# Optimization experiments

Hardware: AMD Instinct MI355X
Metric: run time of the kernel (lower is better)

The kernel has to match this reference:

```python
import jax, jax.numpy as jnp
import numpy as np

NUM_HEADS = 12
LOCAL_WINDOW = 7


def setup_inputs() -> dict:
    key = jax.random.key(0)
    k1, k2, k3 = jax.random.split(key, 3)
    B, N, C = 2, 2048, 768
    x = jax.random.normal(k1, (B, N, C), dtype=jnp.float32)
    w_qkv = jax.random.normal(k2, (3 * C, C), dtype=jnp.float32) * (C ** -0.5)
    w_proj = jax.random.normal(k3, (C, C), dtype=jnp.float32) * (C ** -0.5)
    b_proj = jnp.zeros((C,), dtype=jnp.float32)
    return {"x": x, "w_qkv": w_qkv, "w_proj": w_proj, "b_proj": b_proj}


def reference(x, w_qkv, w_proj, b_proj):
    B, N, C = x.shape
    H = NUM_HEADS
    Dh = C // H
    scale = Dh ** -0.5
    # local-window additive mask: 0 within |i-j|<=w, -inf outside (vectorized)
    idx = jnp.arange(N)
    local_mask = jnp.where(
        jnp.abs(idx[:, None] - idx[None, :]) <= LOCAL_WINDOW, 0.0, -jnp.inf
    ).astype(x.dtype)
    qkv = x @ w_qkv.T
    qkv = qkv.reshape(B, N, 3, H, Dh).transpose(2, 0, 3, 1, 4)
    q, k, v = qkv[0], qkv[1], qkv[2]
    attn = jnp.einsum("bhnd,bhmd->bhnm", q, k) * scale
    attn = attn + local_mask[None, None, :, :]
    attn = jax.nn.softmax(attn, axis=-1)
    out = jnp.einsum("bhnm,bhmd->bhnd", attn, v)
    out = out.transpose(0, 2, 1, 3).reshape(B, N, C)
    return out @ w_proj.T + b_proj
```

## Files before the change

### kernel.cpp

```cpp
#include <hip/hip_runtime.h>
#include <hip/hip_bf16.h>

typedef __bf16 bf16;
typedef bf16 bf16x4 __attribute__((ext_vector_type(4)));
typedef bf16 bf16x8 __attribute__((ext_vector_type(8)));
typedef float floatx4 __attribute__((ext_vector_type(4)));

#define GLOBAL_AS __attribute__((address_space(1)))
#define LDS_AS __attribute__((address_space(3)))

__global__ __launch_bounds__(256)
void cvt3_f32_bf16(const float* __restrict__ s0, const float* __restrict__ s1,
                   const float* __restrict__ s2, bf16* __restrict__ d0,
                   bf16* __restrict__ d1, bf16* __restrict__ d2,
                   int n0, int n1, int n2)
{
    int t = blockIdx.x * blockDim.x + threadIdx.x;
    const float* s; bf16* d; int i;
    if (t < n0)                { s = s0; d = d0; i = t; }
    else if (t < n0 + n1)      { s = s1; d = d1; i = t - n0; }
    else if (t < n0 + n1 + n2) { s = s2; d = d2; i = t - n0 - n1; }
    else return;
    float4 v = ((const float4*)s)[i];
    bf16x4 o = { (bf16)v.x, (bf16)v.y, (bf16)v.z, (bf16)v.w };
    ((bf16x4*)d)[i] = o;
}

template<typename CT, bool AF32, bool WF32, int TM, int M, int N, int K,
         int LDA, int LDC>
__global__ __launch_bounds__(256, 2)
void gemm_bt(const void* __restrict__ Av, const void* __restrict__ Wv,
             CT* __restrict__ C, const float* __restrict__ bias)
{
    constexpr int MI = TM / 32;
    __shared__ __align__(16) bf16 As[TM * 32];
    __shared__ __align__(16) bf16 Bs[128 * 32];

    const int tid  = threadIdx.x;
    const int lane = tid & 63;
    const int wave = tid >> 6;
    const int row0 = blockIdx.x * TM;
    const int col0 = blockIdx.y * 128;

    const int wm = (wave & 1) * (TM / 2);
    const int wn = (wave >> 1) * 64;

    floatx4 acc[MI][4] = {};

    const int fr = lane & 15;
    const int fk = (lane >> 4) * 8;

    const int lr = lane >> 2;
    const int lk = (lane & 3) * 8;

    for (int k0 = 0; k0 < K; k0 += 32) {
        if (AF32) {
            constexpr int NV = TM * 4;
            #pragma unroll
            for (int c = 0; c < NV / 256; ++c) {
                const int idx = tid + c * 256;
                const int r   = idx >> 2;
                const int cb  = (idx & 3) * 8;
                const float4* g = (const float4*)((const float*)Av
                                   + (size_t)(row0 + r) * LDA + k0 + cb);
                float4 g0 = g[0], g1 = g[1];
                bf16x8 va;
                va[0]=(bf16)g0.x; va[1]=(bf16)g0.y; va[2]=(bf16)g0.z; va[3]=(bf16)g0.w;
                va[4]=(bf16)g1.x; va[5]=(bf16)g1.y; va[6]=(bf16)g1.z; va[7]=(bf16)g1.w;
                *(bf16x8*)(As + r * 32 + cb) = va;
            }
        } else {
            constexpr int CAW = TM / 64;
            #pragma unroll
            for (int c = 0; c < CAW; ++c) {
                const int chunk = wave * CAW + c;
                const int r = chunk * 16 + lr;
                const bf16* gA = (const bf16*)Av + (size_t)(row0 + r) * LDA + k0 + lk;
                __builtin_amdgcn_global_load_lds((const GLOBAL_AS void*)gA,
                                                 (LDS_AS void*)(As + chunk * 512),
                                                 16, 0, 0);
            }
        }
        if (WF32) {
            #pragma unroll
            for (int c = 0; c < 2; ++c) {
                const int idx = tid + c * 256;
                const int r   = idx >> 2;
                const int cb  = (idx & 3) * 8;
                const float4* g = (const float4*)((const float*)Wv
                                   + (size_t)(col0 + r) * K + k0 + cb);
                float4 g0 = g[0], g1 = g[1];
                bf16x8 vw;
                vw[0]=(bf16)g0.x; vw[1]=(bf16)g0.y; vw[2]=(bf16)g0.z; vw[3]=(bf16)g0.w;
                vw[4]=(bf16)g1.x; vw[5]=(bf16)g1.y; vw[6]=(bf16)g1.z; vw[7]=(bf16)g1.w;
                *(bf16x8*)(Bs + r * 32 + cb) = vw;
            }
        } else {
            #pragma unroll
            for (int c = 0; c < 2; ++c) {
                const int chunk = wave * 2 + c;
                const int r = chunk * 16 + lr;
                const bf16* gB = (const bf16*)Wv + (size_t)(col0 + r) * K + k0 + lk;
                __builtin_amdgcn_global_load_lds((const GLOBAL_AS void*)gB,
                                                 (LDS_AS void*)(Bs + chunk * 512),
                                                 16, 0, 0);
            }
        }
        __syncthreads();

        bf16x8 af[MI], bfr[4];
        #pragma unroll
        for (int i = 0; i < MI; ++i)
            af[i]  = *(const bf16x8*)(As + (wm + i * 16 + fr) * 32 + fk);
        #pragma unroll
        for (int j = 0; j < 4; ++j)
            bfr[j] = *(const bf16x8*)(Bs + (wn + j * 16 + fr) * 32 + fk);
        #pragma unroll
        for (int i = 0; i < MI; ++i)
            #pragma unroll
            for (int j = 0; j < 4; ++j)
                acc[i][j] = __builtin_amdgcn_mfma_f32_16x16x32_bf16(
                    af[i], bfr[j], acc[i][j], 0, 0, 0);

        __syncthreads();
    }

    const int fc  = lane & 15;
    const int fr4 = (lane >> 4) * 4;
    #pragma unroll
    for (int i = 0; i < MI; ++i) {
        #pragma unroll
        for (int j = 0; j < 4; ++j) {
            const int col = col0 + wn + j * 16 + fc;
            const float b = bias ? bias[col] : 0.0f;
            #pragma unroll
            for (int r = 0; r < 4; ++r) {
                const int row = row0 + wm + i * 16 + fr4 + r;
                C[(size_t)row * LDC + col] = (CT)(acc[i][j][r] + b);
            }
        }
    }
}

__global__ __launch_bounds__(256)
void attn_tile(const bf16* __restrict__ qkv, bf16* __restrict__ aout)
{
    __shared__ __align__(16) bf16 Ks[4][32][72];
    __shared__ __align__(16) bf16 Vt[4][64][40];
    __shared__ __align__(16) bf16 Ps[4][16][40];

    const int w    = threadIdx.x >> 6;
    const int lane = threadIdx.x & 63;
    const int c    = lane & 15;
    const int q    = lane >> 4;
    const int wid  = blockIdx.x * 4 + w;
    const int it   = wid & 127;
    const int bh   = wid >> 7;
    const int h    = bh % 12;
    const int b    = bh / 12;
    const int I0   = it * 16;
    const int bbase = b * 2048;
    const int j0   = I0 - 7;

    #pragma unroll
    for (int itr = 0; itr < 4; ++itr) {
        int idx = itr * 64 + lane;
        int row = idx >> 3;
        int dc  = (idx & 7) * 8;
        int jc  = j0 + row; jc = jc < 0 ? 0 : (jc > 2047 ? 2047 : jc);
        const bf16* base = qkv + (size_t)(bbase + jc) * 2304 + h * 64 + dc;
        bf16x8 kv = *(const bf16x8*)(base + 768);
        bf16x8 vv = *(const bf16x8*)(base + 1536);
        *(bf16x8*)(&Ks[w][row][dc]) = kv;
        #pragma unroll
        for (int e = 0; e < 8; ++e) Vt[w][dc + e][row] = vv[e];
    }

    const bf16* qrow = qkv + (size_t)(bbase + I0 + c) * 2304 + h * 64;
    bf16x8 aq0 = *(const bf16x8*)(qrow + q * 8);
    bf16x8 aq1 = *(const bf16x8*)(qrow + 32 + q * 8);

    __syncthreads();

    floatx4 st[2] = {};
    #pragma unroll
    for (int t = 0; t < 2; ++t) {
        bf16x8 k0 = *(const bf16x8*)(&Ks[w][t * 16 + c][q * 8]);
        bf16x8 k1 = *(const bf16x8*)(&Ks[w][t * 16 + c][32 + q * 8]);
        st[t] = __builtin_amdgcn_mfma_f32_16x16x32_bf16(aq0, k0, st[t], 0, 0, 0);
        st[t] = __builtin_amdgcn_mfma_f32_16x16x32_bf16(aq1, k1, st[t], 0, 0, 0);
    }

    float s[2][4];
    #pragma unroll
    for (int t = 0; t < 2; ++t)
        #pragma unroll
        for (int r = 0; r < 4; ++r) {
            int il = q * 4 + r;
            int jl = t * 16 + c;
            int ja = j0 + jl;
            bool valid = (jl >= il) && (jl <= il + 14) && (ja >= 0) && (ja < 2048);
            s[t][r] = valid ? st[t][r] * 0.125f : -1e30f;
        }

    float l[4], p[2][4];
    #pragma unroll
    for (int r = 0; r < 4; ++r) {
        float m2 = fmaxf(s[0][r], s[1][r]);
        #pragma unroll
        for (int mk = 1; mk < 16; mk <<= 1) m2 = fmaxf(m2, __shfl_xor(m2, mk, 64));
        p[0][r] = __expf(s[0][r] - m2);
        p[1][r] = __expf(s[1][r] - m2);
        float l2 = p[0][r] + p[1][r];
        #pragma unroll
        for (int mk = 1; mk < 16; mk <<= 1) l2 += __shfl_xor(l2, mk, 64);
        l[r] = l2;
    }

    #pragma unroll
    for (int r = 0; r < 4; ++r) {
        Ps[w][q * 4 + r][c]      = (bf16)p[0][r];
        Ps[w][q * 4 + r][16 + c] = (bf16)p[1][r];
    }
    __syncthreads();

    bf16x8 ap = *(const bf16x8*)(&Ps[w][c][q * 8]);
    floatx4 ov[4];
    #pragma unroll
    for (int nt = 0; nt < 4; ++nt) {
        bf16x8 vf = *(const bf16x8*)(&Vt[w][nt * 16 + c][q * 8]);
        floatx4 z = {};
        ov[nt] = __builtin_amdgcn_mfma_f32_16x16x32_bf16(ap, vf, z, 0, 0, 0);
    }

    float rl[4];
    #pragma unroll
    for (int r = 0; r < 4; ++r) rl[r] = 1.0f / l[r];
    #pragma unroll
    for (int r = 0; r < 4; ++r) {
        bf16* orow = aout + (size_t)(bbase + I0 + q * 4 + r) * 768 + h * 64;
        #pragma unroll
        for (int nt = 0; nt < 4; ++nt)
            orow[nt * 16 + c] = (bf16)(ov[nt][r] * rl[r]);
    }
}

extern "C" void kernel_launch(void* const* d_in, const int* in_sizes, int n_in,
                              void* d_out, int out_size, void* d_ws, size_t ws_size,
                              hipStream_t stream)
{
    const float* x      = (const float*)d_in[0];
    const float* w_qkv  = (const float*)d_in[1];
    const float* w_proj = (const float*)d_in[2];
    const float* b_proj = (const float*)d_in[3];
    float* out = (float*)d_out;

    bf16* qkv = (bf16*)d_ws;
    const size_t QKV_B  = (size_t)4096 * 2304 * 2;
    const size_t AO_B   = (size_t)4096 * 768 * 2;
    const size_t XB_B   = (size_t)4096 * 768 * 2;
    const size_t WQKV_B = (size_t)2304 * 768 * 2;
    const size_t WPRJ_B = (size_t)768 * 768 * 2;

    if (ws_size >= QKV_B + AO_B + XB_B + WQKV_B + WPRJ_B) {
        bf16* aout = (bf16*)((char*)d_ws + QKV_B);
        bf16* xb   = (bf16*)((char*)aout + AO_B);
        bf16* wqb  = (bf16*)((char*)xb + XB_B);
        bf16* wpb  = (bf16*)((char*)wqb + WQKV_B);

        const int n0 = 4096 * 768 / 4, n1 = 2304 * 768 / 4, n2 = 768 * 768 / 4;
        cvt3_f32_bf16<<<dim3((n0 + n1 + n2) / 256), 256, 0, stream>>>(
            x, w_qkv, w_proj, xb, wqb, wpb, n0, n1, n2);

        gemm_bt<bf16, false, false, 128, 4096, 2304, 768, 768, 2304>
            <<<dim3(32, 18), 256, 0, stream>>>(xb, wqb, qkv, nullptr);

        attn_tile<<<dim3(768), 256, 0, stream>>>(qkv, aout);

        gemm_bt<float, false, false, 64, 4096, 768, 768, 768, 768>
            <<<dim3(64, 6), 256, 0, stream>>>(aout, wpb, out, b_proj);
    } else {
        gemm_bt<bf16, true, true, 128, 4096, 2304, 768, 768, 2304>
            <<<dim3(32, 18), 256, 0, stream>>>(x, w_qkv, qkv, nullptr);

        bf16* aout = (bf16*)((char*)d_ws + QKV_B);
        attn_tile<<<dim3(768), 256, 0, stream>>>(qkv, aout);

        gemm_bt<float, false, true, 64, 4096, 768, 768, 768, 768>
            <<<dim3(64, 6), 256, 0, stream>>>(aout, w_proj, out, b_proj);
    }
}
```

Before: 122.9 us.

## Fuse convert, QKV GEMM, attention and projection into one cooperative persistent kernel

Replaces the four separate launches with a single cooperative kernel of 512 blocks. Each block loops over the tiles of each phase in turn, with grid-wide syncs between phases, to remove kernel launch gaps and tail idle time between stages. The attention phase now reads K fragments straight from global memory instead of staging them in LDS, and drops its block-wide barriers because each wave uses only its own LDS slice. In exchange it adds grid.sync overhead, and the QKV GEMM's 576 tiles do not split evenly over 512 blocks; the old four-kernel path remains as a fallback if the cooperative launch fails.

```diff
diff --git a/kernel.cpp b/kernel.cpp
--- a/kernel.cpp
+++ b/kernel.cpp
@@ -1,5 +1,8 @@
 #include <hip/hip_runtime.h>
 #include <hip/hip_bf16.h>
+#include <hip/hip_cooperative_groups.h>
+
+namespace cg = cooperative_groups;
 
 typedef __bf16 bf16;
 typedef bf16 bf16x4 __attribute__((ext_vector_type(4)));
@@ -9,102 +12,63 @@
 #define GLOBAL_AS __attribute__((address_space(1)))
 #define LDS_AS __attribute__((address_space(3)))
 
-__global__ __launch_bounds__(256)
-void cvt3_f32_bf16(const float* __restrict__ s0, const float* __restrict__ s1,
-                   const float* __restrict__ s2, bf16* __restrict__ d0,
-                   bf16* __restrict__ d1, bf16* __restrict__ d2,
-                   int n0, int n1, int n2)
-{
-    int t = blockIdx.x * blockDim.x + threadIdx.x;
-    const float* s; bf16* d; int i;
-    if (t < n0)                { s = s0; d = d0; i = t; }
-    else if (t < n0 + n1)      { s = s1; d = d1; i = t - n0; }
-    else if (t < n0 + n1 + n2) { s = s2; d = d2; i = t - n0 - n1; }
-    else return;
-    float4 v = ((const float4*)s)[i];
-    bf16x4 o = { (bf16)v.x, (bf16)v.y, (bf16)v.z, (bf16)v.w };
-    ((bf16x4*)d)[i] = o;
-}
-
-template<typename CT, bool AF32, bool WF32, int TM, int M, int N, int K,
-         int LDA, int LDC>
-__global__ __launch_bounds__(256, 2)
-void gemm_bt(const void* __restrict__ Av, const void* __restrict__ Wv,
-             CT* __restrict__ C, const float* __restrict__ bias)
+__device__ __forceinline__
+void cvt_phase(const float* __restrict__ s0, const float* __restrict__ s1,
+               const float* __restrict__ s2, bf16* __restrict__ d0,
+               bf16* __restrict__ d1, bf16* __restrict__ d2,
+               int n0, int n1, int n2)
+{
+    const int total = n0 + n1 + n2;
+    for (int t = blockIdx.x * 256 + threadIdx.x; t < total;
+         t += gridDim.x * 256) {
+        const float* s; bf16* d; int i;
+        if (t < n0)           { s = s0; d = d0; i = t; }
+        else if (t < n0 + n1) { s = s1; d = d1; i = t - n0; }
+        else                  { s = s2; d = d2; i = t - n0 - n1; }
+        float4 v = ((const float4*)s)[i];
+        bf16x4 o = { (bf16)v.x, (bf16)v.y, (bf16)v.z, (bf16)v.w };
+        ((bf16x4*)d)[i] = o;
+    }
+}
+
+template<typename CT, int TM, int K, int LDA, int LDC>
+__device__ __forceinline__
+void gemm_tile(const bf16* __restrict__ A, const bf16* __restrict__ W,
+               CT* __restrict__ C, const float* __restrict__ bias,
+               bf16* As, bf16* Bs, int row0, int col0)
 {
     constexpr int MI = TM / 32;
-    __shared__ __align__(16) bf16 As[TM * 32];
-    __shared__ __align__(16) bf16 Bs[128 * 32];
-
     const int tid  = threadIdx.x;
     const int lane = tid & 63;
     const int wave = tid >> 6;
-    const int row0 = blockIdx.x * TM;
-    const int col0 = blockIdx.y * 128;
-
     const int wm = (wave & 1) * (TM / 2);
     const int wn = (wave >> 1) * 64;
 
     floatx4 acc[MI][4] = {};
-
     const int fr = lane & 15;
     const int fk = (lane >> 4) * 8;
-
     const int lr = lane >> 2;
     const int lk = (lane & 3) * 8;
 
     for (int k0 = 0; k0 < K; k0 += 32) {
-        if (AF32) {
-            constexpr int NV = TM * 4;
-            #pragma unroll
-            for (int c = 0; c < NV / 256; ++c) {
-                const int idx = tid + c * 256;
-                const int r   = idx >> 2;
-                const int cb  = (idx & 3) * 8;
-                const float4* g = (const float4*)((const float*)Av
-                                   + (size_t)(row0 + r) * LDA + k0 + cb);
-                float4 g0 = g[0], g1 = g[1];
-                bf16x8 va;
-                va[0]=(bf16)g0.x; va[1]=(bf16)g0.y; va[2]=(bf16)g0.z; va[3]=(bf16)g0.w;
-                va[4]=(bf16)g1.x; va[5]=(bf16)g1.y; va[6]=(bf16)g1.z; va[7]=(bf16)g1.w;
-                *(bf16x8*)(As + r * 32 + cb) = va;
-            }
-        } else {
-            constexpr int CAW = TM / 64;
-            #pragma unroll
-            for (int c = 0; c < CAW; ++c) {
-                const int chunk = wave * CAW + c;
-                const int r = chunk * 16 + lr;
-                const bf16* gA = (const bf16*)Av + (size_t)(row0 + r) * LDA + k0 + lk;
-                __builtin_amdgcn_global_load_lds((const GLOBAL_AS void*)gA,
-                                                 (LDS_AS void*)(As + chunk * 512),
-                                                 16, 0, 0);
-            }
+        constexpr int CAW = TM / 64;
+        #pragma unroll
+        for (int c = 0; c < CAW; ++c) {
+            const int chunk = wave * CAW + c;
+            const int r = chunk * 16 + lr;
+            const bf16* gA = A + (size_t)(row0 + r) * LDA + k0 + lk;
+            __builtin_amdgcn_global_load_lds((const GLOBAL_AS void*)gA,
+                                             (LDS_AS void*)(As + chunk * 512),
+                                             16, 0, 0);
         }
-        if (WF32) {
-            #pragma unroll
-            for (int c = 0; c < 2; ++c) {
-                const int idx = tid + c * 256;
-                const int r   = idx >> 2;
-                const int cb  = (idx & 3) * 8;
-                const float4* g = (const float4*)((const float*)Wv
-                                   + (size_t)(col0 + r) * K + k0 + cb);
-                float4 g0 = g[0], g1 = g[1];
-                bf16x8 vw;
-                vw[0]=(bf16)g0.x; vw[1]=(bf16)g0.y; vw[2]=(bf16)g0.z; vw[3]=(bf16)g0.w;
-                vw[4]=(bf16)g1.x; vw[5]=(bf16)g1.y; vw[6]=(bf16)g1.z; vw[7]=(bf16)g1.w;
-                *(bf16x8*)(Bs + r * 32 + cb) = vw;
-            }
-        } else {
-            #pragma unroll
-            for (int c = 0; c < 2; ++c) {
-                const int chunk = wave * 2 + c;
-                const int r = chunk * 16 + lr;
-                const bf16* gB = (const bf16*)Wv + (size_t)(col0 + r) * K + k0 + lk;
-                __builtin_amdgcn_global_load_lds((const GLOBAL_AS void*)gB,
-                                                 (LDS_AS void*)(Bs + chunk * 512),
-                                                 16, 0, 0);
-            }
+        #pragma unroll
+        for (int c = 0; c < 2; ++c) {
+            const int chunk = wave * 2 + c;
+            const int r = chunk * 16 + lr;
+            const bf16* gB = W + (size_t)(col0 + r) * K + k0 + lk;
+            __builtin_amdgcn_global_load_lds((const GLOBAL_AS void*)gB,
+                                             (LDS_AS void*)(Bs + chunk * 512),
+                                             16, 0, 0);
         }
         __syncthreads();
 
@@ -142,18 +106,15 @@
     }
 }
 
-__global__ __launch_bounds__(256)
-void attn_tile(const bf16* __restrict__ qkv, bf16* __restrict__ aout)
-{
-    __shared__ __align__(16) bf16 Ks[4][32][72];
-    __shared__ __align__(16) bf16 Vt[4][64][40];
-    __shared__ __align__(16) bf16 Ps[4][16][40];
-
+__device__ __forceinline__
+void attn_block(const bf16* __restrict__ qkv, bf16* __restrict__ aout,
+                char* smem, int blk)
+{
     const int w    = threadIdx.x >> 6;
     const int lane = threadIdx.x & 63;
     const int c    = lane & 15;
     const int q    = lane >> 4;
-    const int wid  = blockIdx.x * 4 + w;
+    const int wid  = blk * 4 + w;
     const int it   = wid & 127;
     const int bh   = wid >> 7;
     const int h    = bh % 12;
@@ -162,31 +123,32 @@
     const int bbase = b * 2048;
     const int j0   = I0 - 7;
 
+    bf16* Vt = (bf16*)smem           + w * (64 * 40);
+    bf16* Ps = (bf16*)(smem + 20480) + w * (16 * 40);
+
     #pragma unroll
     for (int itr = 0; itr < 4; ++itr) {
         int idx = itr * 64 + lane;
         int row = idx >> 3;
         int dc  = (idx & 7) * 8;
         int jc  = j0 + row; jc = jc < 0 ? 0 : (jc > 2047 ? 2047 : jc);
-        const bf16* base = qkv + (size_t)(bbase + jc) * 2304 + h * 64 + dc;
-        bf16x8 kv = *(const bf16x8*)(base + 768);
-        bf16x8 vv = *(const bf16x8*)(base + 1536);
-        *(bf16x8*)(&Ks[w][row][dc]) = kv;
-        #pragma unroll
-        for (int e = 0; e < 8; ++e) Vt[w][dc + e][row] = vv[e];
+        bf16x8 vv = *(const bf16x8*)(qkv + (size_t)(bbase + jc) * 2304
+                                     + 1536 + h * 64 + dc);
+        #pragma unroll
+        for (int e = 0; e < 8; ++e) Vt[(dc + e) * 40 + row] = vv[e];
     }
 
     const bf16* qrow = qkv + (size_t)(bbase + I0 + c) * 2304 + h * 64;
     bf16x8 aq0 = *(const bf16x8*)(qrow + q * 8);
     bf16x8 aq1 = *(const bf16x8*)(qrow + 32 + q * 8);
 
-    __syncthreads();
-
     floatx4 st[2] = {};
     #pragma unroll
     for (int t = 0; t < 2; ++t) {
-        bf16x8 k0 = *(const bf16x8*)(&Ks[w][t * 16 + c][q * 8]);
-        bf16x8 k1 = *(const bf16x8*)(&Ks[w][t * 16 + c][32 + q * 8]);
+        int jc = j0 + t * 16 + c; jc = jc < 0 ? 0 : (jc > 2047 ? 2047 : jc);
+        const bf16* krow = qkv + (size_t)(bbase + jc) * 2304 + 768 + h * 64;
+        bf16x8 k0 = *(const bf16x8*)(krow + q * 8);
+        bf16x8 k1 = *(const bf16x8*)(krow + 32 + q * 8);
         st[t] = __builtin_amdgcn_mfma_f32_16x16x32_bf16(aq0, k0, st[t], 0, 0, 0);
         st[t] = __builtin_amdgcn_mfma_f32_16x16x32_bf16(aq1, k1, st[t], 0, 0, 0);
     }
@@ -219,16 +181,15 @@
 
     #pragma unroll
     for (int r = 0; r < 4; ++r) {
-        Ps[w][q * 4 + r][c]      = (bf16)p[0][r];
-        Ps[w][q * 4 + r][16 + c] = (bf16)p[1][r];
-    }
-    __syncthreads();
-
-    bf16x8 ap = *(const bf16x8*)(&Ps[w][c][q * 8]);
+        Ps[(q * 4 + r) * 40 + c]      = (bf16)p[0][r];
+        Ps[(q * 4 + r) * 40 + 16 + c] = (bf16)p[1][r];
+    }
+
+    bf16x8 ap = *(const bf16x8*)(&Ps[c * 40 + q * 8]);
     floatx4 ov[4];
     #pragma unroll
     for (int nt = 0; nt < 4; ++nt) {
-        bf16x8 vf = *(const bf16x8*)(&Vt[w][nt * 16 + c][q * 8]);
+        bf16x8 vf = *(const bf16x8*)(&Vt[(nt * 16 + c) * 40 + q * 8]);
         floatx4 z = {};
         ov[nt] = __builtin_amdgcn_mfma_f32_16x16x32_bf16(ap, vf, z, 0, 0, 0);
     }
@@ -243,6 +204,69 @@
         for (int nt = 0; nt < 4; ++nt)
             orow[nt * 16 + c] = (bf16)(ov[nt][r] * rl[r]);
     }
+}
+
+struct FArgs {
+    const float* x; const float* wq; const float* wp; const float* bp;
+    float* out; bf16* qkv; bf16* aout; bf16* xb; bf16* wqb; bf16* wpb;
+};
+
+__global__ __launch_bounds__(256, 2)
+void fused(FArgs a)
+{
+    __shared__ __align__(16) char smem[25600];
+    bf16* As = (bf16*)smem;
+    bf16* Bs = (bf16*)(smem + 8192);
+    cg::grid_group grid = cg::this_grid();
+
+    cvt_phase(a.x, a.wq, a.wp, a.xb, a.wqb, a.wpb, 786432, 442368, 147456);
+    __threadfence();
+    grid.sync();
+
+    for (int t = blockIdx.x; t < 576; t += gridDim.x)
+        gemm_tile<bf16, 128, 768, 768, 2304>(a.xb, a.wqb, a.qkv, nullptr,
+                                             As, Bs, (t & 31) * 128, (t >> 5) * 128);
+    __threadfence();
+    grid.sync();
+
+    for (int t = blockIdx.x; t < 768; t += gridDim.x)
+        attn_block(a.qkv, a.aout, smem, t);
+    __threadfence();
+    grid.sync();
+
+    for (int t = blockIdx.x; t < 384; t += gridDim.x)
+        gemm_tile<float, 64, 768, 768, 768>(a.aout, a.wpb, a.out, a.bp,
+                                            As, Bs, (t & 63) * 64, (t >> 6) * 128);
+}
+
+__global__ __launch_bounds__(256)
+void cvt3_k(const float* s0, const float* s1, const float* s2,
+            bf16* d0, bf16* d1, bf16* d2)
+{ cvt_phase(s0, s1, s2, d0, d1, d2, 786432, 442368, 147456); }
+
+__global__ __launch_bounds__(256, 2)
+void gemm1_k(const bf16* A, const bf16* W, bf16* C)
+{
+    __shared__ __align__(16) bf16 As[128 * 32];
+    __shared__ __align__(16) bf16 Bs[128 * 32];
+    gemm_tile<bf16, 128, 768, 768, 2304>(A, W, C, nullptr, As, Bs,
+                                         blockIdx.x * 128, blockIdx.y * 128);
+}
+
+__global__ __launch_bounds__(256)
+void attn_k(const bf16* qkv, bf16* aout)
+{
+    __shared__ __align__(16) char smem[25600];
+    attn_block(qkv, aout, smem, blockIdx.x);
+}
+
+__global__ __launch_bounds__(256, 2)
+void gemm2_k(const bf16* A, const bf16* W, float* C, const float* bias)
+{
+    __shared__ __align__(16) bf16 As[64 * 32];
+    __shared__ __align__(16) bf16 Bs[128 * 32];
+    gemm_tile<float, 64, 768, 768, 768>(A, W, C, bias, As, Bs,
+                                        blockIdx.x * 64, blockIdx.y * 128);
 }
 
 extern "C" void kernel_launch(void* const* d_in, const int* in_sizes, int n_in,
@@ -255,38 +279,23 @@
     const float* b_proj = (const float*)d_in[3];
     float* out = (float*)d_out;
 
-    bf16* qkv = (bf16*)d_ws;
-    const size_t QKV_B  = (size_t)4096 * 2304 * 2;
-    const size_t AO_B   = (size_t)4096 * 768 * 2;
-    const size_t XB_B   = (size_t)4096 * 768 * 2;
-    const size_t WQKV_B = (size_t)2304 * 768 * 2;
-    const size_t WPRJ_B = (size_t)768 * 768 * 2;
-
-    if (ws_size >= QKV_B + AO_B + XB_B + WQKV_B + WPRJ_B) {
-        bf16* aout = (bf16*)((char*)d_ws + QKV_B);
-        bf16* xb   = (bf16*)((char*)aout + AO_B);
-        bf16* wqb  = (bf16*)((char*)xb + XB_B);
-        bf16* wpb  = (bf16*)((char*)wqb + WQKV_B);
-
-        const int n0 = 4096 * 768 / 4, n1 = 2304 * 768 / 4, n2 = 768 * 768 / 4;
-        cvt3_f32_bf16<<<dim3((n0 + n1 + n2) / 256), 256, 0, stream>>>(
-            x, w_qkv, w_proj, xb, wqb, wpb, n0, n1, n2);
-
-        gemm_bt<bf16, false, false, 128, 4096, 2304, 768, 768, 2304>
-            <<<dim3(32, 18), 256, 0, stream>>>(xb, wqb, qkv, nullptr);
-
-        attn_tile<<<dim3(768), 256, 0, stream>>>(qkv, aout);
-
-        gemm_bt<float, false, false, 64, 4096, 768, 768, 768, 768>
-            <<<dim3(64, 6), 256, 0, stream>>>(aout, wpb, out, b_proj);
-    } else {
-        gemm_bt<bf16, true, true, 128, 4096, 2304, 768, 768, 2304>
-            <<<dim3(32, 18), 256, 0, stream>>>(x, w_qkv, qkv, nullptr);
-
-        bf16* aout = (bf16*)((char*)d_ws + QKV_B);
-        attn_tile<<<dim3(768), 256, 0, stream>>>(qkv, aout);
-
-        gemm_bt<float, false, true, 64, 4096, 768, 768, 768, 768>
-            <<<dim3(64, 6), 256, 0, stream>>>(aout, w_proj, out, b_proj);
-    }
-}
+    bf16* qkv  = (bf16*)d_ws;
+    bf16* aout = qkv  + (size_t)4096 * 2304;
+    bf16* xb   = aout + (size_t)4096 * 768;
+    bf16* wqb  = xb   + (size_t)4096 * 768;
+    bf16* wpb  = wqb  + (size_t)2304 * 768;
+
+    bool done = false;
+    FArgs a{ x, w_qkv, w_proj, b_proj, out, qkv, aout, xb, wqb, wpb };
+    void* params[] = { (void*)&a };
+    if (hipLaunchCooperativeKernel((void*)fused, dim3(512), dim3(256),
+                                   params, 0, stream) == hipSuccess)
+        done = true;
+
+    if (!done) {
+        cvt3_k<<<dim3(5376), 256, 0, stream>>>(x, w_qkv, w_proj, xb, wqb, wpb);
+        gemm1_k<<<dim3(32, 18), 256, 0, stream>>>(xb, wqb, qkv);
+        attn_k<<<dim3(768), 256, 0, stream>>>(qkv, aout);
+        gemm2_k<<<dim3(64, 6), 256, 0, stream>>>(aout, wpb, out, b_proj);
+    }
+}
```

Result: slower. 480.4 us (+291.0%).
